# Kernel optimization log

Hardware: AMD Instinct MI355X
Metric: run time of the kernel (lower is better)

The kernel has to match this reference:

```python
import jax, jax.numpy as jnp
import numpy as np

HIDDEN = 1024
NUM_HEADS = 16
HEAD_DIM = HIDDEN // NUM_HEADS
ROPE_BASE = 10000.0
LN_EPS = 1e-8


def _rope_cos_sin(seq_len, dim, dtype=jnp.float32):
    inv_freq = 1.0 / (ROPE_BASE ** (jnp.arange(0, dim, 2, dtype=jnp.float32) / dim))
    t = jnp.arange(seq_len, dtype=jnp.float32)
    freqs = jnp.einsum('i,j->ij', t, inv_freq)          # [S, dim/2]
    emb = jnp.concatenate([freqs, freqs], axis=-1)       # [S, dim]
    return jnp.cos(emb).astype(dtype), jnp.sin(emb).astype(dtype)


def _rotate_half(x):
    x1, x2 = jnp.split(x, 2, axis=-1)
    return jnp.concatenate([-x2, x1], axis=-1)


def setup_inputs() -> dict:
    key = jax.random.key(0)
    ks = jax.random.split(key, 8)
    B, S, H = 4, 2048, HIDDEN
    x = jax.random.normal(ks[0], (B, S, H), dtype=jnp.float32)
    # causal mask, True = attend
    attn_mask = jnp.tril(jnp.ones((S, S), dtype=bool))[None].repeat(B, axis=0)
    lim_p = 1.0 / np.sqrt(H)
    Wp = jax.random.uniform(ks[1], (H, 4 * H), minval=-lim_p, maxval=lim_p, dtype=jnp.float32)
    bp = jax.random.uniform(ks[2], (4 * H,), minval=-lim_p, maxval=lim_p, dtype=jnp.float32)
    ln_g = jnp.ones((H,), dtype=jnp.float32)
    ln_b = jnp.zeros((H,), dtype=jnp.float32)
    Wt = jax.random.uniform(ks[3], (H, H), minval=-lim_p, maxval=lim_p, dtype=jnp.float32)
    bt = jax.random.uniform(ks[4], (H,), minval=-lim_p, maxval=lim_p, dtype=jnp.float32)
    return {"x": x, "attn_mask": attn_mask, "Wp": Wp, "bp": bp,
            "ln_g": ln_g, "ln_b": ln_b, "Wt": Wt, "bt": bt}


def reference(x, attn_mask, Wp, bp, ln_g, ln_b, Wt, bt):
    B, S, H = x.shape
    nh, hd = NUM_HEADS, HEAD_DIM
    proj = x @ Wp + bp                                   # [B,S,4H]
    U, V, Q, K = jnp.split(proj, 4, axis=-1)
    # [B, nh, S, hd]
    Q = Q.reshape(B, S, nh, hd).transpose(0, 2, 1, 3)
    K = K.reshape(B, S, nh, hd).transpose(0, 2, 1, 3)
    V = V.reshape(B, S, nh, hd).transpose(0, 2, 1, 3)
    cos, sin = _rope_cos_sin(S, hd, x.dtype)             # [S, hd]
    Qr = Q * cos + _rotate_half(Q) * sin
    Kr = K * cos + _rotate_half(K) * sin
    scale = hd ** -0.5
    scores = jnp.einsum('bhqd,bhkd->bhqk', Qr, Kr) * scale
    # masked positions -> sigmoid(-inf) == 0; use where for grad safety
    attn = jnp.where(attn_mask[:, None, :, :], jax.nn.sigmoid(scores), 0.0)
    attn_out = jnp.einsum('bhqk,bhkd->bhqd', attn, V)
    attn_out = attn_out.transpose(0, 2, 1, 3).reshape(B, S, H)
    mu = jnp.mean(attn_out, axis=-1, keepdims=True)
    var = jnp.var(attn_out, axis=-1, keepdims=True)
    attn_out = (attn_out - mu) / jnp.sqrt(var + LN_EPS) * ln_g + ln_b
    gated = jax.nn.silu(U) * attn_out
    out = gated @ Wt + bt
    return x + out
```

## Files before the change

### kernel.cpp

```cpp
#include <hip/hip_runtime.h>
#include <math.h>

#define H 1024
#define NH 16
#define HD 64
#define B_ 4
#define S_ 2048
#define ROWS (B_*S_)

#define QSCALE (-0.1803368801111664f)
#define ROPE_C (9.210340371976184f / 32.0f)

typedef __bf16 bf16x2_t __attribute__((ext_vector_type(2)));
typedef __bf16 bf16x4_t __attribute__((ext_vector_type(4)));
typedef __bf16 bf16x8_t __attribute__((ext_vector_type(8)));
typedef float floatx4_t __attribute__((ext_vector_type(4)));
typedef float floatx16_t __attribute__((ext_vector_type(16)));

#define GLOAD_LDS16(gp, lp)                                                        \
    __builtin_amdgcn_global_load_lds(                                              \
        (const __attribute__((address_space(1))) unsigned int*)(gp),               \
        (__attribute__((address_space(3))) unsigned int*)(lp), 16, 0, 0)

__global__ __launch_bounds__(256)
void prep_kernel(const float* __restrict__ x, const float* __restrict__ Wp,
                 const float* __restrict__ Wt,
                 __bf16* __restrict__ Ax, __bf16* __restrict__ Wp_t,
                 __bf16* __restrict__ Wt_t)
{
    __shared__ __bf16 t[32][33];
    const int flat = blockIdx.x;
    const int tid = threadIdx.x;

    if (flat < 8192) {
        size_t i = (size_t)flat * 256 + tid;
        float4 v = *reinterpret_cast<const float4*>(&x[i * 4]);
        bf16x4_t w = { (__bf16)v.x, (__bf16)v.y, (__bf16)v.z, (__bf16)v.w };
        *reinterpret_cast<bf16x4_t*>(&Ax[i * 4]) = w;
        return;
    }
    const float* W; __bf16* Wo; int K, N, bn, bk;
    if (flat < 12288) {
        int id = flat - 8192;  W = Wp; Wo = Wp_t; K = 1024; N = 4096;
        bn = (id & 127) * 32;  bk = (id >> 7) * 32;
    } else {
        int id = flat - 12288; W = Wt; Wo = Wt_t; K = 1024; N = 1024;
        bn = (id & 31) * 32;   bk = (id >> 5) * 32;
    }
    const int tx = tid & 31, ty = tid >> 5;
#pragma unroll
    for (int i = 0; i < 4; i++) {
        int r = ty + i * 8;
        t[tx][r] = (__bf16)W[(size_t)(bk + r) * N + bn + tx];
    }
    __syncthreads();
#pragma unroll
    for (int i = 0; i < 4; i++) {
        int r = ty + i * 8;
        Wo[(size_t)(bn + r) * K + bk + tx] = t[r][tx];
    }
}


#define MIN15(x) ((x) < 15 ? (x) : 15)

#define STAGE_A(buf, h, tile) do { int _kb = (tile) * 64 + (h) * 32;               \
        char* _lb = lwA + ((buf) * 2 + (h)) * 16384;                               \
        GLOAD_LDS16(a_src0 + _kb, _lb);                                            \
        GLOAD_LDS16(a_src1 + _kb, _lb + 1024); } while (0)
#define STAGE_B(buf, h, tile) do { int _kb = (tile) * 64 + (h) * 32;               \
        char* _lb = lwB + ((buf) * 2 + (h)) * 16384;                               \
        GLOAD_LDS16(b_src0 + _kb, _lb);                                            \
        GLOAD_LDS16(b_src1 + _kb, _lb + 1024); } while (0)

__global__ __launch_bounds__(512, 2)
void gemm_proj(const __bf16* __restrict__ A, const __bf16* __restrict__ Bt,
               const float* __restrict__ bias,
               __bf16* __restrict__ Ug, __bf16* __restrict__ Vh,
               __bf16* __restrict__ Qh, __bf16* __restrict__ Kh)
{
    __shared__ __attribute__((aligned(16))) char smem[131072];

    const int tid  = threadIdx.x;
    const int wave = tid >> 6, lane = tid & 63;
    const int ln15 = lane & 15, q4 = lane >> 4;
    const int wm = wave & 1, wn = wave >> 1;
    const int m0 = blockIdx.y * 256, n0 = blockIdx.x * 256;

    const int srow0 = wave * 32 + (lane >> 2);
    const int csrc  = (lane & 3) ^ ((lane >> 3) & 3);
    const __bf16* a_src0 = A  + (size_t)(m0 + srow0) * 1024 + csrc * 8;
    const __bf16* a_src1 = a_src0 + (size_t)16 * 1024;
    const __bf16* b_src0 = Bt + (size_t)(n0 + srow0) * 1024 + csrc * 8;
    const __bf16* b_src1 = b_src0 + (size_t)16 * 1024;
    char* lwA = smem + wave * 2048;
    char* lwB = smem + 65536 + wave * 2048;

    const int sl = (ln15 >> 1) & 3;
    const int a_lane = (wm * 128 + ln15) * 64 + ((q4 ^ sl) << 4);
    const int b_lane = (wn * 64  + ln15) * 64 + ((q4 ^ sl) << 4);

    floatx4_t acc[8][4];
#pragma unroll
    for (int i = 0; i < 8; i++)
#pragma unroll
        for (int j = 0; j < 4; j++) acc[i][j] = (floatx4_t){0.f, 0.f, 0.f, 0.f};

    STAGE_B(0, 0, 0); STAGE_A(0, 0, 0); STAGE_B(0, 1, 0); STAGE_A(0, 1, 0);
    STAGE_B(1, 0, 1); STAGE_A(1, 0, 1); STAGE_B(1, 1, 1);
    asm volatile("s_waitcnt vmcnt(6)" ::: "memory");
    __builtin_amdgcn_s_barrier();

    bf16x8_t bfr[4];

    for (int it = 0; it < 8; ++it) {
        const int T = 2 * it;
#pragma unroll
        for (int p = 0; p < 8; ++p) {
            const int buf = p >> 2, sub = p & 3, mh = sub & 1, kk = sub >> 1;
            const char* asl = smem + (buf * 2 + kk) * 16384;
            const char* bsl = smem + 65536 + (buf * 2 + kk) * 16384;

            if ((sub & 1) == 0) {
#pragma unroll
                for (int nf = 0; nf < 4; nf++)
                    bfr[nf] = *reinterpret_cast<const bf16x8_t*>(bsl + b_lane + nf * 1024);
            }
            bf16x8_t af[4];
#pragma unroll
            for (int mfi = 0; mfi < 4; mfi++)
                af[mfi] = *reinterpret_cast<const bf16x8_t*>(asl + a_lane + (mh * 4 + mfi) * 1024);

            if      (p == 0) STAGE_A(1, 1, MIN15(T + 1));
            else if (p == 1) STAGE_B(0, 0, MIN15(T + 2));
            else if (p == 2) STAGE_A(0, 0, MIN15(T + 2));
            else if (p == 3) STAGE_B(0, 1, MIN15(T + 2));
            else if (p == 4) STAGE_A(0, 1, MIN15(T + 2));
            else if (p == 5) STAGE_B(1, 0, MIN15(T + 3));
            else if (p == 6) STAGE_A(1, 0, MIN15(T + 3));
            else             STAGE_B(1, 1, MIN15(T + 3));

            if (p == 3 || p == 7)
                asm volatile("s_waitcnt vmcnt(6)" ::: "memory");
            __builtin_amdgcn_s_barrier();

            __builtin_amdgcn_s_setprio(1);
#pragma unroll
            for (int nf = 0; nf < 4; nf++)
#pragma unroll
                for (int mfi = 0; mfi < 4; mfi++)
                    acc[mh * 4 + mfi][nf] = __builtin_amdgcn_mfma_f32_16x16x32_bf16(
                        af[mfi], bfr[nf], acc[mh * 4 + mfi][nf], 0, 0, 0);
            __builtin_amdgcn_s_setprio(0);
            __builtin_amdgcn_s_barrier();
        }
    }
    asm volatile("s_waitcnt vmcnt(0)" ::: "memory");

    const int colbase = n0 + wn * 64;
    float bv[4];
#pragma unroll
    for (int nf = 0; nf < 4; nf++) bv[nf] = bias[colbase + nf * 16 + ln15];

    const int rowb = m0 + wm * 128 + q4 * 4;

    if (n0 < 1024) {
#pragma unroll
        for (int mf = 0; mf < 8; mf++)
#pragma unroll
            for (int nf = 0; nf < 4; nf++) {
                int col = colbase + nf * 16 + ln15;
#pragma unroll
                for (int reg = 0; reg < 4; reg++) {
                    int row = rowb + mf * 16 + reg;
                    Ug[(size_t)row * 1024 + col] = (__bf16)(acc[mf][nf][reg] + bv[nf]);
                }
            }
    } else if (n0 < 2048) {
        const int h = ((n0 - 1024) >> 6) + wn;
#pragma unroll
        for (int mf = 0; mf < 8; mf++)
#pragma unroll
            for (int reg = 0; reg < 4; reg++) {
                int row = rowb + mf * 16 + reg;
                int b = row >> 11, s = row & (S_ - 1);
                size_t orow = ((size_t)(b * NH + h) * S_ + s) * 64;
#pragma unroll
                for (int nf = 0; nf < 4; nf++)
                    Vh[orow + nf * 16 + ln15] = (__bf16)(acc[mf][nf][reg] + bv[nf]);
            }
    } else {
        const bool isQ = (n0 < 3072);
        const int h = ((n0 - (isQ ? 2048 : 3072)) >> 6) + wn;
        __bf16* dst = isQ ? Qh : Kh;
        const float sc = isQ ? QSCALE : 1.0f;
        float inv[2];
        inv[0] = __expf(-(float)(ln15)      * ROPE_C);
        inv[1] = __expf(-(float)(16 + ln15) * ROPE_C);
#pragma unroll
        for (int mf = 0; mf < 8; mf++)
#pragma unroll
            for (int reg = 0; reg < 4; reg++) {
                int row = rowb + mf * 16 + reg;
                int b = row >> 11, s = row & (S_ - 1);
                size_t orow = ((size_t)(b * NH + h) * S_ + s) * 64;
#pragma unroll
                for (int nf = 0; nf < 2; nf++) {
                    float sn, cs;
                    __sincosf((float)s * inv[nf], &sn, &cs);
                    float lo = acc[mf][nf][reg]     + bv[nf];
                    float hi = acc[mf][nf + 2][reg] + bv[nf + 2];
                    int d = nf * 16 + ln15;
                    dst[orow + d]      = (__bf16)((lo * cs - hi * sn) * sc);
                    dst[orow + 32 + d] = (__bf16)((hi * cs + lo * sn) * sc);
                }
            }
    }
}

__global__ __launch_bounds__(256)
void gemm_out(const __bf16* __restrict__ A, const __bf16* __restrict__ Bt,
              const float* __restrict__ bias, const float* __restrict__ resid,
              float* __restrict__ C, int M, int N, int K)
{
    __shared__ __bf16 As[128 * 32];
    __shared__ __bf16 Bs[128 * 32];

    const int tid  = threadIdx.x;
    const int wave = tid >> 6, lane = tid & 63;
    const int l31 = lane & 31, half = lane >> 5;
    const int wm = wave & 1, wn = wave >> 1;
    const int m0 = blockIdx.y * 128, n0 = blockIdx.x * 128;

    const int srow = lane >> 2;
    const int skc  = (((lane & 3) ^ ((srow >> 1) & 3)) * 8);

    const int fsw = (l31 >> 1) & 3;
    int aoff[2][2], boff[2][2];
#pragma unroll
    for (int mt = 0; mt < 2; mt++)
#pragma unroll
        for (int ks = 0; ks < 2; ks++) {
            int ra = wm * 64 + mt * 32 + l31;
            int rb = wn * 64 + mt * 32 + l31;
            int c = ks * 2 + half;
            aoff[mt][ks] = ra * 32 + ((c ^ fsw) * 8);
            boff[mt][ks] = rb * 32 + ((c ^ fsw) * 8);
        }

    floatx16_t acc[2][2];
#pragma unroll
    for (int i = 0; i < 2; i++)
#pragma unroll
        for (int j = 0; j < 2; j++) acc[i][j] = (floatx16_t)(0.f);

    for (int k0 = 0; k0 < K; k0 += 32) {
#pragma unroll
        for (int p = 0; p < 2; p++) {
            int i = wave * 2 + p;
            int rl = i * 16 + srow;
            GLOAD_LDS16(A  + (size_t)(m0 + rl) * K + k0 + skc, &As[i * 512]);
            GLOAD_LDS16(Bt + (size_t)(n0 + rl) * K + k0 + skc, &Bs[i * 512]);
        }
        __syncthreads();

        bf16x8_t af[2][2], bf[2][2];
#pragma unroll
        for (int mt = 0; mt < 2; mt++)
#pragma unroll
            for (int ks = 0; ks < 2; ks++) {
                af[mt][ks] = *reinterpret_cast<const bf16x8_t*>(&As[aoff[mt][ks]]);
                bf[mt][ks] = *reinterpret_cast<const bf16x8_t*>(&Bs[boff[mt][ks]]);
            }
#pragma unroll
        for (int ks = 0; ks < 2; ks++)
#pragma unroll
            for (int mt = 0; mt < 2; mt++)
#pragma unroll
                for (int nt = 0; nt < 2; nt++)
                    acc[mt][nt] = __builtin_amdgcn_mfma_f32_32x32x16_bf16(
                        af[mt][ks], bf[nt][ks], acc[mt][nt], 0, 0, 0);
        __syncthreads();
    }

#pragma unroll
    for (int mt = 0; mt < 2; mt++) {
#pragma unroll
        for (int nt = 0; nt < 2; nt++) {
            int col = n0 + wn * 64 + nt * 32 + l31;
            float bv = bias[col];
#pragma unroll
            for (int reg = 0; reg < 16; reg++) {
                int rowf = (reg & 3) + 8 * (reg >> 2) + 4 * half;
                int row = m0 + wm * 64 + mt * 32 + rowf;
                C[(size_t)row * N + col] = acc[mt][nt][reg] + bv + resid[(size_t)row * N + col];
            }
        }
    }
}

__global__ __launch_bounds__(256)
void transpose_v(const __bf16* __restrict__ Vh, __bf16* __restrict__ VtG)
{
    const int tid = threadIdx.x;
    const int st = blockIdx.x, bh = blockIdx.y;
    const int s0 = st * 64;
    const int d = tid & 63, k16 = tid >> 6;
    __bf16 vals[16];
#pragma unroll
    for (int j = 0; j < 16; j++) {
        int k = s0 + k16 * 16 + j;
        vals[j] = Vh[((size_t)bh * S_ + k) * 64 + d];
    }
    size_t orow = ((size_t)(bh * 64 + d)) * S_ + s0 + k16 * 16;
    *reinterpret_cast<bf16x8_t*>(&VtG[orow])     = *reinterpret_cast<bf16x8_t*>(&vals[0]);
    *reinterpret_cast<bf16x8_t*>(&VtG[orow + 8]) = *reinterpret_cast<bf16x8_t*>(&vals[8]);
}

__global__ __launch_bounds__(512, 4)
void attn_mfma(const __bf16* __restrict__ Qh, const __bf16* __restrict__ Kh,
               const __bf16* __restrict__ VtG, __bf16* __restrict__ attn_out)
{
    __shared__ __bf16 Ks[2][4096];
    __shared__ __bf16 Vt[2][4096];
    __shared__ __bf16 Ps[8][16][72];

    const int tid = threadIdx.x, wave = tid >> 6, lane = tid & 63;
    const int quad = lane >> 4, ln = lane & 15;
    const int p  = blockIdx.x >> 6;
    const int hb = blockIdx.x & 63, h = hb & 15, b = hb >> 4, bh = b * NH + h;

    const int sr = lane >> 3, scl = (lane & 7) ^ sr;
    const size_t khead = (size_t)bh * S_ * 64;
    const int koff = (wave * 8 + sr) * 64 + scl * 8;
    const size_t vg = ((size_t)bh * 64 + wave * 8 + sr) * S_ + scl * 8;

    const int m7 = ln & 7;
    int ka[4][2];
#pragma unroll
    for (int nt = 0; nt < 4; nt++) {
        int row = nt * 16 + ln;
        ka[nt][0] = row * 64 + ((quad ^ m7) << 3);
        ka[nt][1] = row * 64 + (((quad + 4) ^ m7) << 3);
    }

    const int wl   = wave * 16 + ln;
    const int wl63 = wl & 63;
    const bool hiw = wave >= 4;

    for (int hf = 0; hf < 2; hf++) {
        const int qt = hf ? p : (15 - p);
        const int Q0 = qt * 128, T0 = 2 * qt;

        const size_t qr = ((size_t)bh * S_ + Q0 + wl) * 64;
        const bf16x8_t qa0 = *reinterpret_cast<const bf16x8_t*>(&Qh[qr + quad * 8]);
        const bf16x8_t qa1 = *reinterpret_cast<const bf16x8_t*>(&Qh[qr + 32 + quad * 8]);

        floatx4_t o[4];
#pragma unroll
        for (int dt = 0; dt < 4; dt++) o[dt] = (floatx4_t){0.f, 0.f, 0.f, 0.f};

        GLOAD_LDS16(Kh  + khead + koff, &Ks[0][wave * 512]);
        GLOAD_LDS16(VtG + vg,           &Vt[0][wave * 512]);

        for (int kt = 0; kt <= T0 + 1; kt++) {
            const int buf = kt & 1;
            __syncthreads();
            if (kt <= T0) {
                const int nb = buf ^ 1;
                GLOAD_LDS16(Kh  + khead + (size_t)(kt + 1) * 4096 + koff, &Ks[nb][wave * 512]);
                GLOAD_LDS16(VtG + vg + (kt + 1) * 64,                      &Vt[nb][wave * 512]);
            }

            const int rel = kt - T0;
            const int mode = (rel < 0) ? 0 : (rel == 0 ? (hiw ? 0 : 1) : (hiw ? 1 : 2));
            if (mode == 2) continue;

            bf16x8_t kf[4][2];
#pragma unroll
            for (int nt = 0; nt < 4; nt++) {
                kf[nt][0] = *reinterpret_cast<const bf16x8_t*>(&Ks[buf][ka[nt][0]]);
                kf[nt][1] = *reinterpret_cast<const bf16x8_t*>(&Ks[buf][ka[nt][1]]);
            }

            floatx4_t st[4];
#pragma unroll
            for (int nt = 0; nt < 4; nt++) {
                floatx4_t acc = (floatx4_t){0.f, 0.f, 0.f, 0.f};
                acc = __builtin_amdgcn_mfma_f32_16x16x32_bf16(kf[nt][0], qa0, acc, 0, 0, 0);
                acc = __builtin_amdgcn_mfma_f32_16x16x32_bf16(kf[nt][1], qa1, acc, 0, 0, 0);
                st[nt] = acc;
            }

#pragma unroll
            for (int nt = 0; nt < 4; nt++) {
                bf16x4_t pk;
#pragma unroll
                for (int r = 0; r < 4; r++) {
                    float a = st[nt][r];
                    if (mode == 1) {
                        int kl = nt * 16 + quad * 4 + r;
                        a = (kl <= wl63) ? a : __builtin_inff();
                    }
                    float pv = __builtin_amdgcn_rcpf(1.f + __builtin_amdgcn_exp2f(a));
                    pk[r] = (__bf16)pv;
                }
                *reinterpret_cast<bf16x4_t*>(&Ps[wave][ln][nt * 16 + quad * 4]) = pk;
            }

            bf16x8_t vf[4][2];
#pragma unroll
            for (int dt = 0; dt < 4; dt++) {
                vf[dt][0] = *reinterpret_cast<const bf16x8_t*>(&Vt[buf][ka[dt][0]]);
                vf[dt][1] = *reinterpret_cast<const bf16x8_t*>(&Vt[buf][ka[dt][1]]);
            }

            const __bf16* prow = &Ps[wave][ln][quad * 8];
            bf16x8_t p0 = *reinterpret_cast<const bf16x8_t*>(prow);
            bf16x8_t p1 = *reinterpret_cast<const bf16x8_t*>(prow + 32);
#pragma unroll
            for (int dt = 0; dt < 4; dt++) {
                o[dt] = __builtin_amdgcn_mfma_f32_16x16x32_bf16(p0, vf[dt][0], o[dt], 0, 0, 0);
                o[dt] = __builtin_amdgcn_mfma_f32_16x16x32_bf16(p1, vf[dt][1], o[dt], 0, 0, 0);
            }
        }

        const int qrow_g = b * S_ + Q0 + wave * 16 + quad * 4;
#pragma unroll
        for (int dt = 0; dt < 4; dt++) {
#pragma unroll
            for (int reg = 0; reg < 4; reg++) {
                attn_out[(size_t)(qrow_g + reg) * H + h * 64 + dt * 16 + ln] =
                    (__bf16)o[dt][reg];
            }
        }
    }
}

__global__ __launch_bounds__(256)
void ln_gate_kernel(const __bf16* __restrict__ attn_out, const __bf16* __restrict__ Ug,
                    const float* __restrict__ ln_g, const float* __restrict__ ln_b,
                    __bf16* __restrict__ gated)
{
    const int row = blockIdx.x;
    const int tid = threadIdx.x;

    bf16x4_t vb = *reinterpret_cast<const bf16x4_t*>(&attn_out[(size_t)row * H + tid * 4]);
    float v0 = (float)vb[0], v1 = (float)vb[1], v2 = (float)vb[2], v3 = (float)vb[3];
    float s  = v0 + v1 + v2 + v3;
    float sq = v0 * v0 + v1 * v1 + v2 * v2 + v3 * v3;
#pragma unroll
    for (int off = 32; off > 0; off >>= 1) {
        s  += __shfl_down(s, off);
        sq += __shfl_down(sq, off);
    }
    __shared__ float ps[4], pq[4];
    int wave = tid >> 6, lane = tid & 63;
    if (lane == 0) { ps[wave] = s; pq[wave] = sq; }
    __syncthreads();
    float ts = ps[0] + ps[1] + ps[2] + ps[3];
    float tq = pq[0] + pq[1] + pq[2] + pq[3];
    float mu  = ts * (1.f / (float)H);
    float var = tq * (1.f / (float)H) - mu * mu;
    float rstd = rsqrtf(var + 1e-8f);

    bf16x4_t ub = *reinterpret_cast<const bf16x4_t*>(&Ug[(size_t)row * 1024 + tid * 4]);
    float4 g  = *reinterpret_cast<const float4*>(&ln_g[tid * 4]);
    float4 bb = *reinterpret_cast<const float4*>(&ln_b[tid * 4]);
    float u0 = (float)ub[0], u1 = (float)ub[1], u2 = (float)ub[2], u3 = (float)ub[3];
    bf16x4_t outv;
    outv[0] = (__bf16)(((v0 - mu) * rstd * g.x + bb.x) * (u0 / (1.f + __expf(-u0))));
    outv[1] = (__bf16)(((v1 - mu) * rstd * g.y + bb.y) * (u1 / (1.f + __expf(-u1))));
    outv[2] = (__bf16)(((v2 - mu) * rstd * g.z + bb.z) * (u2 / (1.f + __expf(-u2))));
    outv[3] = (__bf16)(((v3 - mu) * rstd * g.w + bb.w) * (u3 / (1.f + __expf(-u3))));
    *reinterpret_cast<bf16x4_t*>(&gated[(size_t)row * H + tid * 4]) = outv;
}

extern "C" void kernel_launch(void* const* d_in, const int* in_sizes, int n_in,
                              void* d_out, int out_size, void* d_ws, size_t ws_size,
                              hipStream_t stream)
{
    const float* x    = (const float*)d_in[0];
    const float* Wp   = (const float*)d_in[2];
    const float* bp   = (const float*)d_in[3];
    const float* ln_g = (const float*)d_in[4];
    const float* ln_b = (const float*)d_in[5];
    const float* Wt   = (const float*)d_in[6];
    const float* bt   = (const float*)d_in[7];
    float* out = (float*)d_out;

    char* ws = (char*)d_ws;
    const size_t MB = 1024 * 1024;
    __bf16* Ug    = (__bf16*)(ws);
    __bf16* Vh    = (__bf16*)(ws + 16  * MB);
    __bf16* Qh    = (__bf16*)(ws + 32  * MB);
    __bf16* Kh    = (__bf16*)(ws + 48  * MB);
    __bf16* attn  = (__bf16*)(ws + 64  * MB);
    __bf16* gated = (__bf16*)(ws + 80  * MB);
    __bf16* VtG   = (__bf16*)(ws + 96  * MB);
    __bf16* Ax    = (__bf16*)(ws + 112 * MB);
    __bf16* Wp_t  = (__bf16*)(ws + 128 * MB);
    __bf16* Wt_t  = (__bf16*)(ws + 136 * MB);

    prep_kernel<<<13312, 256, 0, stream>>>(x, Wp, Wt, Ax, Wp_t, Wt_t);

    dim3 g1(4096 / 256, ROWS / 256);
    gemm_proj<<<g1, 512, 0, stream>>>(Ax, Wp_t, bp, Ug, Vh, Qh, Kh);

    transpose_v<<<dim3(S_ / 64, B_ * NH), 256, 0, stream>>>(Vh, VtG);

    attn_mfma<<<8 * B_ * NH, 512, 0, stream>>>(Qh, Kh, VtG, attn);

    ln_gate_kernel<<<ROWS, 256, 0, stream>>>(attn, Ug, ln_g, ln_b, gated);

    dim3 g3(1024 / 128, ROWS / 128);
    gemm_out<<<g3, 256, 0, stream>>>(gated, Wt_t, bt, x, out, ROWS, 1024, 1024);
}
```

Measured before the change: 325.1 us.

## Shrink projection GEMM tile to 128x256 with simple double-buffer and remapped grid

Replaces the 256x256-tile, 128KB-LDS, eight-phase interleaved pipeline in the projection GEMM with a 128x256 tile, a K-step of 32 and a plain two-buffer LDS scheme (48KB). Launch bounds go to 4 blocks per CU, and a 1D grid of 1024 blocks is remapped so that consecutive blocks share B columns, for better L2 reuse. The aim is higher occupancy and simpler scheduling. The cost is less reuse per tile, a full vmcnt(0) wait plus barrier on every K-step, and less overlap between loads and MFMA.

```diff
diff --git a/kernel.cpp b/kernel.cpp
--- a/kernel.cpp
+++ b/kernel.cpp
@@ -62,111 +62,91 @@
 }
 
 
-#define MIN15(x) ((x) < 15 ? (x) : 15)
-
-#define STAGE_A(buf, h, tile) do { int _kb = (tile) * 64 + (h) * 32;               \
-        char* _lb = lwA + ((buf) * 2 + (h)) * 16384;                               \
-        GLOAD_LDS16(a_src0 + _kb, _lb);                                            \
-        GLOAD_LDS16(a_src1 + _kb, _lb + 1024); } while (0)
-#define STAGE_B(buf, h, tile) do { int _kb = (tile) * 64 + (h) * 32;               \
-        char* _lb = lwB + ((buf) * 2 + (h)) * 16384;                               \
-        GLOAD_LDS16(b_src0 + _kb, _lb);                                            \
-        GLOAD_LDS16(b_src1 + _kb, _lb + 1024); } while (0)
-
-__global__ __launch_bounds__(512, 2)
+#define PSTAGE_A(tile, nb) GLOAD_LDS16(a_src + (size_t)(tile) * 32, &As[nb][wave * 512])
+#define PSTAGE_B(tile, nb) do {                                                     \
+        GLOAD_LDS16(b_src0 + (size_t)(tile) * 32, &Bs[nb][wave * 512]);             \
+        GLOAD_LDS16(b_src1 + (size_t)(tile) * 32, &Bs[nb][4096 + wave * 512]); } while (0)
+
+__global__ __launch_bounds__(512, 4)
 void gemm_proj(const __bf16* __restrict__ A, const __bf16* __restrict__ Bt,
                const float* __restrict__ bias,
                __bf16* __restrict__ Ug, __bf16* __restrict__ Vh,
                __bf16* __restrict__ Qh, __bf16* __restrict__ Kh)
 {
-    __shared__ __attribute__((aligned(16))) char smem[131072];
+    __shared__ __attribute__((aligned(16))) __bf16 As[2][128 * 32];
+    __shared__ __attribute__((aligned(16))) __bf16 Bs[2][256 * 32];
 
     const int tid  = threadIdx.x;
     const int wave = tid >> 6, lane = tid & 63;
     const int ln15 = lane & 15, q4 = lane >> 4;
     const int wm = wave & 1, wn = wave >> 1;
-    const int m0 = blockIdx.y * 256, n0 = blockIdx.x * 256;
-
-    const int srow0 = wave * 32 + (lane >> 2);
-    const int csrc  = (lane & 3) ^ ((lane >> 3) & 3);
-    const __bf16* a_src0 = A  + (size_t)(m0 + srow0) * 1024 + csrc * 8;
-    const __bf16* a_src1 = a_src0 + (size_t)16 * 1024;
-    const __bf16* b_src0 = Bt + (size_t)(n0 + srow0) * 1024 + csrc * 8;
-    const __bf16* b_src1 = b_src0 + (size_t)16 * 1024;
-    char* lwA = smem + wave * 2048;
-    char* lwB = smem + 65536 + wave * 2048;
-
-    const int sl = (ln15 >> 1) & 3;
-    const int a_lane = (wm * 128 + ln15) * 64 + ((q4 ^ sl) << 4);
-    const int b_lane = (wn * 64  + ln15) * 64 + ((q4 ^ sl) << 4);
-
-    floatx4_t acc[8][4];
-#pragma unroll
-    for (int i = 0; i < 8; i++)
+
+    const int bid = blockIdx.x;
+    const int wid = (bid & 7) * 128 + (bid >> 3);
+    const int m0 = (wid & 63) * 128;
+    const int n0 = (wid >> 6) * 256;
+
+    const int srow = tid >> 2;
+    const int csrc = (tid & 3) ^ ((tid >> 3) & 3);
+    const __bf16* a_src  = A  + (size_t)(m0 + srow) * 1024 + csrc * 8;
+    const __bf16* b_src0 = Bt + (size_t)(n0 + srow) * 1024 + csrc * 8;
+    const __bf16* b_src1 = b_src0 + (size_t)128 * 1024;
+
+    int aoff[4], boff[4];
+#pragma unroll
+    for (int f = 0; f < 4; f++) {
+        int ra = wm * 64 + f * 16 + ln15;
+        aoff[f] = ra * 32 + ((q4 ^ ((ra >> 1) & 3)) * 8);
+        int rb = wn * 64 + f * 16 + ln15;
+        boff[f] = rb * 32 + ((q4 ^ ((rb >> 1) & 3)) * 8);
+    }
+
+    floatx4_t acc[4][4];
+#pragma unroll
+    for (int i = 0; i < 4; i++)
 #pragma unroll
         for (int j = 0; j < 4; j++) acc[i][j] = (floatx4_t){0.f, 0.f, 0.f, 0.f};
 
-    STAGE_B(0, 0, 0); STAGE_A(0, 0, 0); STAGE_B(0, 1, 0); STAGE_A(0, 1, 0);
-    STAGE_B(1, 0, 1); STAGE_A(1, 0, 1); STAGE_B(1, 1, 1);
-    asm volatile("s_waitcnt vmcnt(6)" ::: "memory");
+    PSTAGE_A(0, 0); PSTAGE_B(0, 0);
+    asm volatile("s_waitcnt vmcnt(0)" ::: "memory");
     __builtin_amdgcn_s_barrier();
 
-    bf16x8_t bfr[4];
-
-    for (int it = 0; it < 8; ++it) {
-        const int T = 2 * it;
-#pragma unroll
-        for (int p = 0; p < 8; ++p) {
-            const int buf = p >> 2, sub = p & 3, mh = sub & 1, kk = sub >> 1;
-            const char* asl = smem + (buf * 2 + kk) * 16384;
-            const char* bsl = smem + 65536 + (buf * 2 + kk) * 16384;
-
-            if ((sub & 1) == 0) {
-#pragma unroll
-                for (int nf = 0; nf < 4; nf++)
-                    bfr[nf] = *reinterpret_cast<const bf16x8_t*>(bsl + b_lane + nf * 1024);
-            }
-            bf16x8_t af[4];
-#pragma unroll
-            for (int mfi = 0; mfi < 4; mfi++)
-                af[mfi] = *reinterpret_cast<const bf16x8_t*>(asl + a_lane + (mh * 4 + mfi) * 1024);
-
-            if      (p == 0) STAGE_A(1, 1, MIN15(T + 1));
-            else if (p == 1) STAGE_B(0, 0, MIN15(T + 2));
-            else if (p == 2) STAGE_A(0, 0, MIN15(T + 2));
-            else if (p == 3) STAGE_B(0, 1, MIN15(T + 2));
-            else if (p == 4) STAGE_A(0, 1, MIN15(T + 2));
-            else if (p == 5) STAGE_B(1, 0, MIN15(T + 3));
-            else if (p == 6) STAGE_A(1, 0, MIN15(T + 3));
-            else             STAGE_B(1, 1, MIN15(T + 3));
-
-            if (p == 3 || p == 7)
-                asm volatile("s_waitcnt vmcnt(6)" ::: "memory");
-            __builtin_amdgcn_s_barrier();
-
-            __builtin_amdgcn_s_setprio(1);
-#pragma unroll
-            for (int nf = 0; nf < 4; nf++)
-#pragma unroll
-                for (int mfi = 0; mfi < 4; mfi++)
-                    acc[mh * 4 + mfi][nf] = __builtin_amdgcn_mfma_f32_16x16x32_bf16(
-                        af[mfi], bfr[nf], acc[mh * 4 + mfi][nf], 0, 0, 0);
-            __builtin_amdgcn_s_setprio(0);
-            __builtin_amdgcn_s_barrier();
-        }
-    }
-    asm volatile("s_waitcnt vmcnt(0)" ::: "memory");
+    for (int T = 0; T < 32; ++T) {
+        const int buf = T & 1, nb = buf ^ 1;
+
+        bf16x8_t bfr[4], af[4];
+#pragma unroll
+        for (int f = 0; f < 4; f++)
+            bfr[f] = *reinterpret_cast<const bf16x8_t*>(&Bs[buf][boff[f]]);
+#pragma unroll
+        for (int f = 0; f < 4; f++)
+            af[f] = *reinterpret_cast<const bf16x8_t*>(&As[buf][aoff[f]]);
+
+        if (T < 31) { PSTAGE_A(T + 1, nb); PSTAGE_B(T + 1, nb); }
+
+        __builtin_amdgcn_s_setprio(1);
+#pragma unroll
+        for (int nf = 0; nf < 4; nf++)
+#pragma unroll
+            for (int mf = 0; mf < 4; mf++)
+                acc[mf][nf] = __builtin_amdgcn_mfma_f32_16x16x32_bf16(
+                    af[mf], bfr[nf], acc[mf][nf], 0, 0, 0);
+        __builtin_amdgcn_s_setprio(0);
+
+        asm volatile("s_waitcnt vmcnt(0)" ::: "memory");
+        __builtin_amdgcn_s_barrier();
+    }
 
     const int colbase = n0 + wn * 64;
     float bv[4];
 #pragma unroll
     for (int nf = 0; nf < 4; nf++) bv[nf] = bias[colbase + nf * 16 + ln15];
 
-    const int rowb = m0 + wm * 128 + q4 * 4;
+    const int rowb = m0 + wm * 64 + q4 * 4;
 
     if (n0 < 1024) {
 #pragma unroll
-        for (int mf = 0; mf < 8; mf++)
+        for (int mf = 0; mf < 4; mf++)
 #pragma unroll
             for (int nf = 0; nf < 4; nf++) {
                 int col = colbase + nf * 16 + ln15;
@@ -179,7 +159,7 @@
     } else if (n0 < 2048) {
         const int h = ((n0 - 1024) >> 6) + wn;
 #pragma unroll
-        for (int mf = 0; mf < 8; mf++)
+        for (int mf = 0; mf < 4; mf++)
 #pragma unroll
             for (int reg = 0; reg < 4; reg++) {
                 int row = rowb + mf * 16 + reg;
@@ -198,7 +178,7 @@
         inv[0] = __expf(-(float)(ln15)      * ROPE_C);
         inv[1] = __expf(-(float)(16 + ln15) * ROPE_C);
 #pragma unroll
-        for (int mf = 0; mf < 8; mf++)
+        for (int mf = 0; mf < 4; mf++)
 #pragma unroll
             for (int reg = 0; reg < 4; reg++) {
                 int row = rowb + mf * 16 + reg;
@@ -504,8 +484,7 @@
 
     prep_kernel<<<13312, 256, 0, stream>>>(x, Wp, Wt, Ax, Wp_t, Wt_t);
 
-    dim3 g1(4096 / 256, ROWS / 256);
-    gemm_proj<<<g1, 512, 0, stream>>>(Ax, Wp_t, bp, Ug, Vh, Qh, Kh);
+    gemm_proj<<<1024, 512, 0, stream>>>(Ax, Wp_t, bp, Ug, Vh, Qh, Kh);
 
     transpose_v<<<dim3(S_ / 64, B_ * NH), 256, 0, stream>>>(Vh, VtG);
 
```

Result: no change. 319.5 us (-1.7%).
